# Kernel optimization log

Measured on AMD Instinct MI355X. Metric: run time of the kernel, lower is better.

## Reference

```python
import jax, jax.numpy as jnp
import numpy as np

# module config (from init_kwargs)
IN_CH, OUT_CH, KSIZE = 32, 64, 1
N_FILTERS = 16          # top-k filters routed per sample
STRIDE, PADDING = 1, 0


def setup_inputs() -> dict:
    key = jax.random.key(0)
    k_x, k_w, k_b, k_rw, k_rb = jax.random.split(key, 5)
    B, H, W = 32, 224, 224
    x = jax.random.normal(k_x, (B, IN_CH, H, W), dtype=jnp.float32)
    # conv params (kaiming-ish scale)
    fan_in = IN_CH * KSIZE * KSIZE
    wb = 1.0 / np.sqrt(fan_in)
    weight = jax.random.uniform(k_w, (OUT_CH, IN_CH, KSIZE, KSIZE), minval=-wb, maxval=wb, dtype=jnp.float32)
    bias = jax.random.uniform(k_b, (OUT_CH,), minval=-wb, maxval=wb, dtype=jnp.float32)
    # router linear: in_channels -> out_channels
    rb = 1.0 / np.sqrt(IN_CH)
    router_w = jax.random.uniform(k_rw, (OUT_CH, IN_CH), minval=-rb, maxval=rb, dtype=jnp.float32)
    router_b = jax.random.uniform(k_rb, (OUT_CH,), minval=-rb, maxval=rb, dtype=jnp.float32)
    return {"x": x, "weight": weight, "bias": bias, "router_w": router_w, "router_b": router_b}


def reference(x, weight, bias, router_w, router_b):
    B = x.shape[0]
    # global average pool -> router logits [B, OUT_CH]
    pooled = x.mean(axis=(2, 3))
    logits = pooled @ router_w.T + router_b
    # per-sample top-k filter selection -> binary channel mask [B, OUT_CH]
    _, top_idx = jax.lax.top_k(logits, N_FILTERS)
    mask = jnp.zeros((B, OUT_CH), dtype=x.dtype).at[jnp.arange(B)[:, None], top_idx].set(1.0)
    # dense conv2d, then gate channels per sample
    out = jax.lax.conv_general_dilated(
        x, weight,
        window_strides=(STRIDE, STRIDE),
        padding=[(PADDING, PADDING), (PADDING, PADDING)],
        dimension_numbers=("NCHW", "OIHW", "NCHW"),
    ) + bias[None, :, None, None]
    return out * mask[:, :, None, None]
```

## Files before the change

### kernel.cpp

```cpp
#include <hip/hip_runtime.h>

#define IN_CH   32
#define OUT_CH  64
#define NFILT   16
#define NINACT  (OUT_CH - NFILT)
#define BATCH   32
#define HW      50176
#define HW4     12544
#define CHUNKS  49

typedef float vfloat4 __attribute__((ext_vector_type(4)));

__global__ __launch_bounds__(256) void pool_kernel(const float* __restrict__ x,
                                                   float* __restrict__ pooled) {
    const int bc = blockIdx.x;
    const float4* xp = reinterpret_cast<const float4*>(x) + (size_t)bc * HW4;

    float4 s = make_float4(0.f, 0.f, 0.f, 0.f);
    for (int i = threadIdx.x; i < HW4; i += 256) {
        float4 v = xp[i];
        s.x += v.x; s.y += v.y; s.z += v.z; s.w += v.w;
    }
    float sum = (s.x + s.y) + (s.z + s.w);

    for (int off = 32; off > 0; off >>= 1)
        sum += __shfl_down(sum, off, 64);

    __shared__ float red[4];
    if ((threadIdx.x & 63) == 0) red[threadIdx.x >> 6] = sum;
    __syncthreads();
    if (threadIdx.x == 0) {
        float t = (red[0] + red[1]) + (red[2] + red[3]);
        pooled[bc] = t * (1.0f / (float)HW);
    }
}

__global__ __launch_bounds__(256) void conv_kernel(const float* __restrict__ x,
                                                   const float* __restrict__ weight,
                                                   const float* __restrict__ bias,
                                                   const float* __restrict__ rw,
                                                   const float* __restrict__ rb,
                                                   const float* __restrict__ pooled,
                                                   float* __restrict__ out) {
    __shared__ float w_s[OUT_CH][IN_CH];
    __shared__ float b_s[OUT_CH];
    __shared__ float lg[OUT_CH];
    __shared__ unsigned char act[OUT_CH];
    __shared__ short alist[NFILT];
    __shared__ short ilist[NINACT];

    const int b     = blockIdx.x / CHUNKS;
    const int chunk = blockIdx.x % CHUNKS;

    for (int i = threadIdx.x; i < OUT_CH * IN_CH; i += 256)
        (&w_s[0][0])[i] = weight[i];

    if (threadIdx.x < OUT_CH) {
        const int o = threadIdx.x;
        b_s[o] = bias[o];
        float acc = rb[o];
        #pragma unroll
        for (int c = 0; c < IN_CH; ++c)
            acc += pooled[b * IN_CH + c] * rw[o * IN_CH + c];
        lg[o] = acc;
    }
    __syncthreads();

    if (threadIdx.x < OUT_CH) {
        const int o = threadIdx.x;
        const float v = lg[o];
        int rank = 0;
        #pragma unroll
        for (int j = 0; j < OUT_CH; ++j) {
            const float lj = lg[j];
            rank += (lj > v) || (lj == v && j < o);
        }
        const bool a = (rank < NFILT);
        act[o] = a;
        if (a) alist[rank] = (short)o;
    }
    __syncthreads();

    if (threadIdx.x < OUT_CH) {
        const int o = threadIdx.x;
        if (!act[o]) {
            int irank = 0;
            for (int j = 0; j < o; ++j) irank += !act[j];
            ilist[irank] = (short)o;
        }
    }
    __syncthreads();

    const int pos = chunk * 256 + threadIdx.x;
    const float4* x4 = reinterpret_cast<const float4*>(x);
    vfloat4*      o4 = reinterpret_cast<vfloat4*>(out);

    float4 xv[IN_CH];
    #pragma unroll
    for (int c = 0; c < IN_CH; ++c)
        xv[c] = x4[(size_t)(b * IN_CH + c) * HW4 + pos];

    const vfloat4 z = {0.f, 0.f, 0.f, 0.f};
    #pragma unroll
    for (int k = 0; k < NINACT; ++k) {
        const int o = ilist[k];
        __builtin_nontemporal_store(z, &o4[(size_t)(b * OUT_CH + o) * HW4 + pos]);
    }

    #pragma unroll
    for (int k = 0; k < NFILT; ++k) {
        const int o = alist[k];
        const float bv = b_s[o];
        vfloat4 r = {bv, bv, bv, bv};
        #pragma unroll
        for (int c = 0; c < IN_CH; ++c) {
            const float w = w_s[o][c];
            r.x += w * xv[c].x;
            r.y += w * xv[c].y;
            r.z += w * xv[c].z;
            r.w += w * xv[c].w;
        }
        __builtin_nontemporal_store(r, &o4[(size_t)(b * OUT_CH + o) * HW4 + pos]);
    }
}

extern "C" void kernel_launch(void* const* d_in, const int* in_sizes, int n_in,
                              void* d_out, int out_size, void* d_ws, size_t ws_size,
                              hipStream_t stream) {
    const float* x    = (const float*)d_in[0];
    const float* w    = (const float*)d_in[1];
    const float* bias = (const float*)d_in[2];
    const float* rw   = (const float*)d_in[3];
    const float* rb   = (const float*)d_in[4];
    float* out    = (float*)d_out;
    float* pooled = (float*)d_ws;

    pool_kernel<<<BATCH * IN_CH, 256, 0, stream>>>(x, pooled);
    conv_kernel<<<BATCH * CHUNKS, 256, 0, stream>>>(x, w, bias, rw, rb, pooled, out);
}
```

Baseline: 124.1 us.

## Fuse pooling and gated conv into one cooperative kernel with grid sync

Replaces the two-launch pool then conv sequence with a single cooperative kernel. It pools all planes, does a grid-wide sync, has every block compute router logits and top-k for all samples, and then runs a grid-stride loop over conv work units. The aim is to remove the kernel launch gap and the tail between the two phases. In exchange it adds a grid barrier, redundant router and top-k work in every block, and a fixed 256x512 grid that may underfill the GPU or lose occupancy from register pressure. The old two-kernel path is kept as a fallback if the cooperative launch fails.

```diff
diff --git a/kernel.cpp b/kernel.cpp
--- a/kernel.cpp
+++ b/kernel.cpp
@@ -1,4 +1,7 @@
 #include <hip/hip_runtime.h>
+#include <hip/hip_cooperative_groups.h>
+
+namespace cg = cooperative_groups;
 
 #define IN_CH   32
 #define OUT_CH  64
@@ -8,31 +11,150 @@
 #define HW      50176
 #define HW4     12544
 #define CHUNKS  49
+#define NPLANE  (BATCH * IN_CH)
+#define NUNITS  (BATCH * CHUNKS)
+#define FGRID   256
+#define FBLOCK  512
+#define NHALF   (FGRID * 2)
 
 typedef float vfloat4 __attribute__((ext_vector_type(4)));
+
+__global__ __launch_bounds__(FBLOCK, 2) void fused_kernel(
+        const float* __restrict__ x,
+        const float* __restrict__ weight,
+        const float* __restrict__ bias,
+        const float* __restrict__ rw,
+        const float* __restrict__ rb,
+        float* __restrict__ pooled,
+        float* __restrict__ out) {
+
+    const int tid  = threadIdx.x;
+    const int half = tid >> 8;
+    const int ht   = tid & 255;
+    const int hid  = blockIdx.x * 2 + half;
+
+    __shared__ float red[2][4];
+    const float4* x4 = reinterpret_cast<const float4*>(x);
+    #pragma unroll
+    for (int rep = 0; rep < 2; ++rep) {
+        const int p = hid + rep * NHALF;
+        const float4* xp = x4 + (size_t)p * HW4;
+        float s = 0.f;
+        for (int i = ht; i < HW4; i += 256) {
+            float4 v = xp[i];
+            s += (v.x + v.y) + (v.z + v.w);
+        }
+        for (int off = 32; off > 0; off >>= 1)
+            s += __shfl_down(s, off, 64);
+        if ((ht & 63) == 0) red[half][ht >> 6] = s;
+        __syncthreads();
+        if (ht == 0)
+            pooled[p] = ((red[half][0] + red[half][1]) +
+                         (red[half][2] + red[half][3])) * (1.0f / (float)HW);
+        __syncthreads();
+    }
+
+    cg::this_grid().sync();
+
+    __shared__ float w_s[OUT_CH][IN_CH];
+    __shared__ float b_s[OUT_CH];
+    __shared__ float lg[BATCH][OUT_CH];
+    __shared__ unsigned char act[BATCH][OUT_CH];
+    __shared__ short alist[BATCH][NFILT];
+    __shared__ short ilist[BATCH][NINACT];
+
+    for (int i = tid; i < OUT_CH * IN_CH; i += FBLOCK)
+        (&w_s[0][0])[i] = weight[i];
+    if (tid < OUT_CH) b_s[tid] = bias[tid];
+
+    for (int p = tid; p < BATCH * OUT_CH; p += FBLOCK) {
+        const int b = p >> 6, o = p & 63;
+        float acc = rb[o];
+        #pragma unroll
+        for (int c = 0; c < IN_CH; ++c)
+            acc += pooled[b * IN_CH + c] * rw[o * IN_CH + c];
+        lg[b][o] = acc;
+    }
+    __syncthreads();
+
+    for (int p = tid; p < BATCH * OUT_CH; p += FBLOCK) {
+        const int b = p >> 6, o = p & 63;
+        const float v = lg[b][o];
+        int rank = 0;
+        #pragma unroll
+        for (int j = 0; j < OUT_CH; ++j) {
+            const float lj = lg[b][j];
+            rank += (lj > v) || (lj == v && j < o);
+        }
+        const bool a = (rank < NFILT);
+        act[b][o] = a;
+        if (a) alist[b][rank] = (short)o;
+    }
+    __syncthreads();
+
+    for (int p = tid; p < BATCH * OUT_CH; p += FBLOCK) {
+        const int b = p >> 6, o = p & 63;
+        if (!act[b][o]) {
+            int irank = 0;
+            for (int j = 0; j < o; ++j) irank += !act[b][j];
+            ilist[b][irank] = (short)o;
+        }
+    }
+    __syncthreads();
+
+    vfloat4* o4 = reinterpret_cast<vfloat4*>(out);
+
+    for (int u = hid; u < NUNITS; u += NHALF) {
+        const int b     = u / CHUNKS;
+        const int chunk = u - b * CHUNKS;
+        const int pos   = chunk * 256 + ht;
+
+        float4 xv[IN_CH];
+        #pragma unroll
+        for (int c = 0; c < IN_CH; ++c)
+            xv[c] = x4[(size_t)(b * IN_CH + c) * HW4 + pos];
+
+        const vfloat4 z = {0.f, 0.f, 0.f, 0.f};
+        #pragma unroll
+        for (int k = 0; k < NINACT; ++k) {
+            const int o = ilist[b][k];
+            __builtin_nontemporal_store(z, &o4[(size_t)(b * OUT_CH + o) * HW4 + pos]);
+        }
+
+        #pragma unroll
+        for (int k = 0; k < NFILT; ++k) {
+            const int o = alist[b][k];
+            const float bv = b_s[o];
+            vfloat4 r = {bv, bv, bv, bv};
+            #pragma unroll
+            for (int c = 0; c < IN_CH; ++c) {
+                const float w = w_s[o][c];
+                r.x += w * xv[c].x;
+                r.y += w * xv[c].y;
+                r.z += w * xv[c].z;
+                r.w += w * xv[c].w;
+            }
+            __builtin_nontemporal_store(r, &o4[(size_t)(b * OUT_CH + o) * HW4 + pos]);
+        }
+    }
+}
 
 __global__ __launch_bounds__(256) void pool_kernel(const float* __restrict__ x,
                                                    float* __restrict__ pooled) {
     const int bc = blockIdx.x;
     const float4* xp = reinterpret_cast<const float4*>(x) + (size_t)bc * HW4;
-
-    float4 s = make_float4(0.f, 0.f, 0.f, 0.f);
+    float s = 0.f;
     for (int i = threadIdx.x; i < HW4; i += 256) {
         float4 v = xp[i];
-        s.x += v.x; s.y += v.y; s.z += v.z; s.w += v.w;
-    }
-    float sum = (s.x + s.y) + (s.z + s.w);
-
+        s += (v.x + v.y) + (v.z + v.w);
+    }
     for (int off = 32; off > 0; off >>= 1)
-        sum += __shfl_down(sum, off, 64);
-
+        s += __shfl_down(s, off, 64);
     __shared__ float red[4];
-    if ((threadIdx.x & 63) == 0) red[threadIdx.x >> 6] = sum;
-    __syncthreads();
-    if (threadIdx.x == 0) {
-        float t = (red[0] + red[1]) + (red[2] + red[3]);
-        pooled[bc] = t * (1.0f / (float)HW);
-    }
+    if ((threadIdx.x & 63) == 0) red[threadIdx.x >> 6] = s;
+    __syncthreads();
+    if (threadIdx.x == 0)
+        pooled[bc] = ((red[0] + red[1]) + (red[2] + red[3])) * (1.0f / (float)HW);
 }
 
 __global__ __launch_bounds__(256) void conv_kernel(const float* __restrict__ x,
@@ -106,7 +228,6 @@
         const int o = ilist[k];
         __builtin_nontemporal_store(z, &o4[(size_t)(b * OUT_CH + o) * HW4 + pos]);
     }
-
     #pragma unroll
     for (int k = 0; k < NFILT; ++k) {
         const int o = alist[k];
@@ -135,6 +256,13 @@
     float* out    = (float*)d_out;
     float* pooled = (float*)d_ws;
 
-    pool_kernel<<<BATCH * IN_CH, 256, 0, stream>>>(x, pooled);
-    conv_kernel<<<BATCH * CHUNKS, 256, 0, stream>>>(x, w, bias, rw, rb, pooled, out);
-}
+    void* args[] = {(void*)&x, (void*)&w, (void*)&bias, (void*)&rw,
+                    (void*)&rb, (void*)&pooled, (void*)&out};
+    hipError_t err = hipLaunchCooperativeKernel((const void*)fused_kernel,
+                                                dim3(FGRID), dim3(FBLOCK),
+                                                args, 0, stream);
+    if (err != hipSuccess) {
+        pool_kernel<<<NPLANE, 256, 0, stream>>>(x, pooled);
+        conv_kernel<<<NUNITS, 256, 0, stream>>>(x, w, bias, rw, rb, pooled, out);
+    }
+}
```

New measurement: 191.4 us. +54.3%, slower.
